# Kernel optimization log

Hardware: AMD Instinct MI355X
Metric: run time of the kernel (lower is better)

The kernel has to match this reference:

```python
import jax, jax.numpy as jnp
import numpy as np

B, T, IN_DIM = 128, 4096, 13
UNITS, MOTOR = 64, 6
LAYERS = [35, 23, 6]   # AutoNCP(64, 6): inter / command / motor neurons
_SPLITS = [35, 58]     # cumulative layer boundaries inside the 64-unit state


def setup_inputs() -> dict:
    keys = iter(jax.random.split(jax.random.key(0), 64))
    def rn(shape, s=0.1):
        return jax.random.normal(next(keys), shape, dtype=jnp.float32) * s
    inp = {"x": jax.random.normal(next(keys), (B, T, IN_DIM), dtype=jnp.float32)}
    # mixed-memory LSTM cell (ncps: input_map has bias, recurrent_map does not)
    inp["lstm_wi"] = rn((4 * UNITS, IN_DIM))
    inp["lstm_wh"] = rn((4 * UNITS, UNITS))
    inp["lstm_b"] = rn((4 * UNITS,))
    # wired CfC layers: ff1/ff2/time_a/time_b acting on concat([input, h])
    in_dims = [IN_DIM] + LAYERS[:-1]
    for i, (d, h) in enumerate(zip(in_dims, LAYERS)):
        for nm in ("w1", "w2", "wa", "wb"):
            inp[f"cfc{i}_{nm}"] = rn((h, d + h))
        for nm in ("b1", "b2", "ba", "bb"):
            inp[f"cfc{i}_{nm}"] = rn((h,))
    inp["gyro_w1"] = rn((32, MOTOR)); inp["gyro_b1"] = rn((32,))
    inp["gyro_w2"] = rn((3, 32));     inp["gyro_b2"] = rn((3,))
    inp["acc_w1"] = rn((32, MOTOR));  inp["acc_b1"] = rn((32,))
    inp["acc_w2"] = rn((3, 32));      inp["acc_b2"] = rn((3,))
    inp["unc_w1"] = rn((16, MOTOR));  inp["unc_b1"] = rn((16,))
    inp["unc_w2"] = rn((6, 16));      inp["unc_b2"] = rn((6,))
    return inp


def _cfc_step(inp, h, p):
    """ncps CfCCell, mode='default', no backbone, ts = 1.0."""
    W1, b1, W2, b2, Wa, ba, Wb, bb = p
    z = jnp.concatenate([inp, h], axis=-1)            # (B, in+hid)
    ff1 = jnp.tanh(z @ W1.T + b1)
    ff2 = jnp.tanh(z @ W2.T + b2)
    t = jax.nn.sigmoid((z @ Wa.T + ba) + (z @ Wb.T + bb))  # t_a*ts + t_b, ts==1
    return ff1 * (1.0 - t) + t * ff2


def reference(x, lstm_wi, lstm_wh, lstm_b,
              cfc0_w1, cfc0_b1, cfc0_w2, cfc0_b2, cfc0_wa, cfc0_ba, cfc0_wb, cfc0_bb,
              cfc1_w1, cfc1_b1, cfc1_w2, cfc1_b2, cfc1_wa, cfc1_ba, cfc1_wb, cfc1_bb,
              cfc2_w1, cfc2_b1, cfc2_w2, cfc2_b2, cfc2_wa, cfc2_ba, cfc2_wb, cfc2_bb,
              gyro_w1, gyro_b1, gyro_w2, gyro_b2,
              acc_w1, acc_b1, acc_w2, acc_b2,
              unc_w1, unc_b1, unc_w2, unc_b2):
    layer_params = (
        (cfc0_w1, cfc0_b1, cfc0_w2, cfc0_b2, cfc0_wa, cfc0_ba, cfc0_wb, cfc0_bb),
        (cfc1_w1, cfc1_b1, cfc1_w2, cfc1_b2, cfc1_wa, cfc1_ba, cfc1_wb, cfc1_bb),
        (cfc2_w1, cfc2_b1, cfc2_w2, cfc2_b2, cfc2_wa, cfc2_ba, cfc2_wb, cfc2_bb),
    )

    def step(carry, xt):  # xt: (B, 13)
        h, c = carry
        # mixed-memory LSTM over the full 64-unit state (forget gate +1.0)
        zg = xt @ lstm_wi.T + lstm_b + h @ lstm_wh.T
        ia, ig, fg, og = jnp.split(zg, 4, axis=-1)
        c_new = c * jax.nn.sigmoid(fg + 1.0) + jnp.tanh(ia) * jax.nn.sigmoid(ig)
        h_lstm = jnp.tanh(c_new) * jax.nn.sigmoid(og)
        # wired CfC: inter -> command -> motor, each fed previous layer's output
        hs = jnp.split(h_lstm, _SPLITS, axis=-1)
        inp = xt
        new_hs = []
        for hi, p in zip(hs, layer_params):
            inp = _cfc_step(inp, hi, p)
            new_hs.append(inp)
        return (jnp.concatenate(new_hs, axis=-1), c_new), inp  # motor out (B,6)

    Bsz = x.shape[0]
    h0 = jnp.zeros((Bsz, UNITS), x.dtype)
    c0 = jnp.zeros((Bsz, UNITS), x.dtype)
    _, outs = jax.lax.scan(step, (h0, c0), jnp.swapaxes(x, 0, 1))
    cfc_out = jnp.swapaxes(outs, 0, 1)  # (B, T, 6)

    gyro = jnp.tanh(cfc_out @ gyro_w1.T + gyro_b1) @ gyro_w2.T + gyro_b2
    acc = jnp.tanh(cfc_out @ acc_w1.T + acc_b1) @ acc_w2.T + acc_b2
    pred = jnp.concatenate([gyro, acc], axis=-1)                      # (B, T, 6)
    unc = jax.nn.softplus(
        jax.nn.relu(cfc_out @ unc_w1.T + unc_b1) @ unc_w2.T + unc_b2)  # (B, T, 6)
    return pred, unc
```

## Files before the change

### kernel.cpp

```cpp
#include <hip/hip_runtime.h>
#include <math.h>

#define BATCH 128
#define TSTEPS 4096
#define INDIM 13
#define XT 64


__device__ __forceinline__ float fsig(float x) {
    return __builtin_amdgcn_rcpf(1.f + __expf(-x));
}
__device__ __forceinline__ float ftanh(float x) {
    float s = fsig(x + x);
    return s + s - 1.f;
}
__device__ __forceinline__ float fsoftplus(float x) {
    return (x > 15.f) ? x : __logf(1.f + __expf(x));
}

__device__ __forceinline__ float qxor1(float v) {
    return __int_as_float(__builtin_amdgcn_update_dpp(
        0, __float_as_int(v), 0xB1, 0xF, 0xF, true));
}
__device__ __forceinline__ float qxor2(float v) {
    return __int_as_float(__builtin_amdgcn_update_dpp(
        0, __float_as_int(v), 0x4E, 0xF, 0xF, true));
}
#define BFLY4(a) { a += qxor1(a); a += qxor2(a); }

#define FMA4(acc, W, q, zv) { acc += zv.x * W##_##q##_0; acc += zv.y * W##_##q##_1; \
                              acc += zv.z * W##_##q##_2; acc += zv.w * W##_##q##_3; }

__global__ __launch_bounds__(256, 1)
void rnn_kernel(const float* __restrict__ x,
                const float* __restrict__ lstm_wi, const float* __restrict__ lstm_wh,
                const float* __restrict__ lstm_b,
                const float* __restrict__ c0w1, const float* __restrict__ c0w2,
                const float* __restrict__ c0wa, const float* __restrict__ c0wb,
                const float* __restrict__ c0b1, const float* __restrict__ c0b2,
                const float* __restrict__ c0ba, const float* __restrict__ c0bb,
                const float* __restrict__ c1w1, const float* __restrict__ c1w2,
                const float* __restrict__ c1wa, const float* __restrict__ c1wb,
                const float* __restrict__ c1b1, const float* __restrict__ c1b2,
                const float* __restrict__ c1ba, const float* __restrict__ c1bb,
                const float* __restrict__ c2w1, const float* __restrict__ c2w2,
                const float* __restrict__ c2wa, const float* __restrict__ c2wb,
                const float* __restrict__ c2b1, const float* __restrict__ c2b2,
                const float* __restrict__ c2ba, const float* __restrict__ c2bb,
                float* __restrict__ out)
{
    const int bb = blockIdx.x;
    const int t  = threadIdx.x;
    const int k  = t & 3;
    const int u  = t >> 2;

    __shared__ __align__(16) float smem[2688];
    float* zL  = smem;
    float* z0  = smem + 96;
    float* z1  = smem + 160;
    float* z2  = smem + 224;
    float* xt0 = smem + 256;
    float* xt1 = smem + 1088;
    float* ot0 = smem + 1920;
    float* ot1 = smem + 2304;

    const long xbase = (long)bb * TSTEPS * INDIM;
    const long obase = (long)bb * TSTEPS * 6;

    auto lwf = [&](int A, int c) -> float {
        int r = A * 64 + u;
        return (c < 13) ? lstm_wi[r * 13 + c]
             : (c < 77) ? lstm_wh[r * 64 + (c - 13)] : 0.f;
    };
#define DEF_WL(A,q) \
    float wl##A##_##q##_0 = lwf(A, 24*k + 4*q + 0); \
    float wl##A##_##q##_1 = lwf(A, 24*k + 4*q + 1); \
    float wl##A##_##q##_2 = lwf(A, 24*k + 4*q + 2); \
    float wl##A##_##q##_3 = lwf(A, 24*k + 4*q + 3);
    DEF_WL(0,0) DEF_WL(0,1) DEF_WL(0,2) DEF_WL(0,3) DEF_WL(0,4) DEF_WL(0,5)
    DEF_WL(1,0) DEF_WL(1,1) DEF_WL(1,2) DEF_WL(1,3) DEF_WL(1,4) DEF_WL(1,5)
    DEF_WL(2,0) DEF_WL(2,1) DEF_WL(2,2) DEF_WL(2,3) DEF_WL(2,4) DEF_WL(2,5)
    DEF_WL(3,0) DEF_WL(3,1) DEF_WL(3,2) DEF_WL(3,3) DEF_WL(3,4) DEF_WL(3,5)
#undef DEF_WL
    const float bL0 = lstm_b[u];
    const float bL1 = lstm_b[64 + u];
    const float bL2 = lstm_b[128 + u];
    const float bL3 = lstm_b[192 + u];

    const int grp  = (u < 35) ? 0 : (u < 58) ? 1 : 2;
    const int row  = (grp == 0) ? u : (grp == 1) ? (u - 35) : (u - 58);
    const int rl   = (grp == 0) ? 48 : (grp == 1) ? 58 : 29;
    const int clen = (grp == 0) ? 12 : (grp == 1) ? 16 : 8;
    const int cb   = clen * k;
    const float *W0p, *W1p, *W2p, *W3p;
    float bC0, bC1, bC2, bC3;
    if (grp == 0) {
        W0p = c0w1 + row * 48; W1p = c0w2 + row * 48;
        W2p = c0wa + row * 48; W3p = c0wb + row * 48;
        bC0 = c0b1[row]; bC1 = c0b2[row]; bC2 = c0ba[row]; bC3 = c0bb[row];
    } else if (grp == 1) {
        W0p = c1w1 + row * 58; W1p = c1w2 + row * 58;
        W2p = c1wa + row * 58; W3p = c1wb + row * 58;
        bC0 = c1b1[row]; bC1 = c1b2[row]; bC2 = c1ba[row]; bC3 = c1bb[row];
    } else {
        W0p = c2w1 + row * 29; W1p = c2w2 + row * 29;
        W2p = c2wa + row * 29; W3p = c2wb + row * 29;
        bC0 = c2b1[row]; bC1 = c2b2[row]; bC2 = c2ba[row]; bC3 = c2bb[row];
    }
    auto cwf = [&](const float* W, int c) -> float {
        int cc = cb + c;
        return (c < clen && cc < rl) ? W[cc] : 0.f;
    };
#define DEF_WC(A,q) \
    float wc##A##_##q##_0 = cwf(W##A##p, 4*q + 0); \
    float wc##A##_##q##_1 = cwf(W##A##p, 4*q + 1); \
    float wc##A##_##q##_2 = cwf(W##A##p, 4*q + 2); \
    float wc##A##_##q##_3 = cwf(W##A##p, 4*q + 3);
    DEF_WC(0,0) DEF_WC(0,1) DEF_WC(0,2) DEF_WC(0,3)
    DEF_WC(1,0) DEF_WC(1,1) DEF_WC(1,2) DEF_WC(1,3)
    DEF_WC(2,0) DEF_WC(2,1) DEF_WC(2,2) DEF_WC(2,3)
    DEF_WC(3,0) DEF_WC(3,1) DEF_WC(3,2) DEF_WC(3,3)
#undef DEF_WC

    float creg = 0.f;

    smem[t] = 0.f;
    if (t < 208) {
        float4 xi = *(const float4*)(x + xbase + 4 * t);
        *(float4*)&xt0[4 * t] = xi;
    }
    if (t < 13) { float x0 = x[xbase + t]; zL[t] = x0; z0[t] = x0; }
    __syncthreads();

    #pragma unroll 1
    for (int ts = 0; ts < TSTEPS; ++ts) {
        const int par = (ts >> 6) & 1;
        const int lts = ts & 63;

        {
            const float4* zc = (const float4*)(zL + 24 * k);
            float4 q0 = zc[0], q1 = zc[1], q2 = zc[2],
                   q3 = zc[3], q4 = zc[4], q5 = zc[5];
            float a0 = 0.f, a1 = 0.f, a2 = 0.f, a3 = 0.f;
            FMA4(a0, wl0, 0, q0) FMA4(a0, wl0, 1, q1) FMA4(a0, wl0, 2, q2)
            FMA4(a0, wl0, 3, q3) FMA4(a0, wl0, 4, q4) FMA4(a0, wl0, 5, q5)
            FMA4(a1, wl1, 0, q0) FMA4(a1, wl1, 1, q1) FMA4(a1, wl1, 2, q2)
            FMA4(a1, wl1, 3, q3) FMA4(a1, wl1, 4, q4) FMA4(a1, wl1, 5, q5)
            FMA4(a2, wl2, 0, q0) FMA4(a2, wl2, 1, q1) FMA4(a2, wl2, 2, q2)
            FMA4(a2, wl2, 3, q3) FMA4(a2, wl2, 4, q4) FMA4(a2, wl2, 5, q5)
            FMA4(a3, wl3, 0, q0) FMA4(a3, wl3, 1, q1) FMA4(a3, wl3, 2, q2)
            FMA4(a3, wl3, 3, q3) FMA4(a3, wl3, 4, q4) FMA4(a3, wl3, 5, q5)
            BFLY4(a0) BFLY4(a1) BFLY4(a2) BFLY4(a3)
            a0 += bL0; a1 += bL1; a2 += bL2; a3 += bL3;
            float cn = creg * fsig(a2 + 1.f) + ftanh(a0) * fsig(a1);
            creg = cn;
            float hl = ftanh(cn) * fsig(a3);
            if (k == 0) {
                if (u < 35)      z0[13 + u] = hl;
                else if (u < 58) z1[u]      = hl;
                else             z2[u - 35] = hl;
            }
        }
        __syncthreads();

        if (grp == 0) {
            const float4* zc = (const float4*)(z0 + 12 * k);
            float4 v0 = zc[0], v1 = zc[1], v2 = zc[2];
            float a0 = 0.f, a1 = 0.f, a2 = 0.f, a3 = 0.f;
            FMA4(a0, wc0, 0, v0) FMA4(a0, wc0, 1, v1) FMA4(a0, wc0, 2, v2)
            FMA4(a1, wc1, 0, v0) FMA4(a1, wc1, 1, v1) FMA4(a1, wc1, 2, v2)
            FMA4(a2, wc2, 0, v0) FMA4(a2, wc2, 1, v1) FMA4(a2, wc2, 2, v2)
            FMA4(a3, wc3, 0, v0) FMA4(a3, wc3, 1, v1) FMA4(a3, wc3, 2, v2)
            BFLY4(a0) BFLY4(a1) BFLY4(a2) BFLY4(a3)
            a0 += bC0; a1 += bC1; a2 += bC2; a3 += bC3;
            float tg = fsig(a2 + a3);
            float f1 = ftanh(a0), f2 = ftanh(a1);
            float o = f1 + tg * (f2 - f1);
            if (k == 0) { z1[row] = o; zL[13 + row] = o; }
        } else {
            if (lts == 62 && (ts + 2) < TSTEPS) {
                int i = (t - 140) * 2;
                float* dst = par ? xt0 : xt1;
                const float* src = x + xbase + (long)(ts + 2) * 13;
                if (i < 208)     *(float4*)&dst[4*i]     = *(const float4*)(src + 4*i);
                if (i + 1 < 208) *(float4*)&dst[4*(i+1)] = *(const float4*)(src + 4*(i+1));
            }
            if (lts == 0 && ts > 0) {
                int i = t - 140;
                if (i < 96) {
                    const float* src = par ? ot0 : ot1;
                    float4 v = *(const float4*)&src[4 * i];
                    *(float4*)(out + obase + (long)(ts - XT) * 6 + 4 * i) = v;
                }
            }
        }
        __syncthreads();

        if (grp == 1) {
            const float4* zc = (const float4*)(z1 + 16 * k);
            float4 v0 = zc[0], v1 = zc[1], v2 = zc[2], v3 = zc[3];
            float a0 = 0.f, a1 = 0.f, a2 = 0.f, a3 = 0.f;
            FMA4(a0, wc0, 0, v0) FMA4(a0, wc0, 1, v1) FMA4(a0, wc0, 2, v2) FMA4(a0, wc0, 3, v3)
            FMA4(a1, wc1, 0, v0) FMA4(a1, wc1, 1, v1) FMA4(a1, wc1, 2, v2) FMA4(a1, wc1, 3, v3)
            FMA4(a2, wc2, 0, v0) FMA4(a2, wc2, 1, v1) FMA4(a2, wc2, 2, v2) FMA4(a2, wc2, 3, v3)
            FMA4(a3, wc3, 0, v0) FMA4(a3, wc3, 1, v1) FMA4(a3, wc3, 2, v2) FMA4(a3, wc3, 3, v3)
            BFLY4(a0) BFLY4(a1) BFLY4(a2) BFLY4(a3)
            a0 += bC0; a1 += bC1; a2 += bC2; a3 += bC3;
            float tg = fsig(a2 + a3);
            float f1 = ftanh(a0), f2 = ftanh(a1);
            float o = f1 + tg * (f2 - f1);
            if (k == 0) { z2[row] = o; zL[48 + row] = o; }
        }
        __syncthreads();

        if (grp == 2) {
            const float4* zc = (const float4*)(z2 + 8 * k);
            float4 v0 = zc[0], v1 = zc[1];
            float a0 = 0.f, a1 = 0.f, a2 = 0.f, a3 = 0.f;
            FMA4(a0, wc0, 0, v0) FMA4(a0, wc0, 1, v1)
            FMA4(a1, wc1, 0, v0) FMA4(a1, wc1, 1, v1)
            FMA4(a2, wc2, 0, v0) FMA4(a2, wc2, 1, v1)
            FMA4(a3, wc3, 0, v0) FMA4(a3, wc3, 1, v1)
            BFLY4(a0) BFLY4(a1) BFLY4(a2) BFLY4(a3)
            a0 += bC0; a1 += bC1; a2 += bC2; a3 += bC3;
            float tg = fsig(a2 + a3);
            float f1 = ftanh(a0), f2 = ftanh(a1);
            float o = f1 + tg * (f2 - f1);
            if (k == 0) {
                zL[71 + row] = o;
                float* ob = par ? ot1 : ot0;
                ob[lts * 6 + row] = o;
            }
        } else if (t < 13 && (ts + 1) < TSTEPS) {
            const float* xb = (((ts + 1) >> 6) & 1) ? xt1 : xt0;
            float xn = xb[((ts + 1) & 63) * 13 + t];
            zL[t] = xn; z0[t] = xn;
        }
        __syncthreads();
    }

    if (t < 96) {
        float4 v = *(const float4*)&ot1[4 * t];
        *(float4*)(out + obase + (long)(TSTEPS - XT) * 6 + 4 * t) = v;
    }
}

#define S_GW1 0
#define S_GB1 192
#define S_GW2 224
#define S_GB2 320
#define S_AW1 323
#define S_AB1 515
#define S_AW2 547
#define S_AB2 643
#define S_UW1 646
#define S_UB1 742
#define S_UW2 758
#define S_UB2 854
#define S_TOT 860

__global__ __launch_bounds__(256)
void head_kernel(const float* __restrict__ gw1, const float* __restrict__ gb1,
                 const float* __restrict__ gw2, const float* __restrict__ gb2,
                 const float* __restrict__ aw1, const float* __restrict__ ab1,
                 const float* __restrict__ aw2, const float* __restrict__ ab2,
                 const float* __restrict__ uw1, const float* __restrict__ ub1,
                 const float* __restrict__ uw2, const float* __restrict__ ub2,
                 float* __restrict__ out)
{
    __shared__ float s[S_TOT];
    const int t = threadIdx.x;
    if (t < 192) { s[S_GW1 + t] = gw1[t]; s[S_AW1 + t] = aw1[t]; }
    if (t < 96)  { s[S_GW2 + t] = gw2[t]; s[S_AW2 + t] = aw2[t];
                   s[S_UW1 + t] = uw1[t]; s[S_UW2 + t] = uw2[t]; }
    if (t < 32)  { s[S_GB1 + t] = gb1[t]; s[S_AB1 + t] = ab1[t]; }
    if (t < 16)  { s[S_UB1 + t] = ub1[t]; }
    if (t < 3)   { s[S_GB2 + t] = gb2[t]; s[S_AB2 + t] = ab2[t]; }
    if (t < 6)   { s[S_UB2 + t] = ub2[t]; }
    __syncthreads();

    const long p = (long)blockIdx.x * 256 + t;
    const long base = p * 6;
    float m0 = out[base+0], m1 = out[base+1], m2 = out[base+2];
    float m3 = out[base+3], m4 = out[base+4], m5 = out[base+5];

    float gy0 = s[S_GB2+0], gy1 = s[S_GB2+1], gy2 = s[S_GB2+2];
    float ac0 = s[S_AB2+0], ac1 = s[S_AB2+1], ac2 = s[S_AB2+2];
    #pragma unroll
    for (int i = 0; i < 32; ++i) {
        float hg = s[S_GB1+i] + s[S_GW1+i*6+0]*m0 + s[S_GW1+i*6+1]*m1
                 + s[S_GW1+i*6+2]*m2 + s[S_GW1+i*6+3]*m3
                 + s[S_GW1+i*6+4]*m4 + s[S_GW1+i*6+5]*m5;
        hg = ftanh(hg);
        gy0 += s[S_GW2+i]*hg; gy1 += s[S_GW2+32+i]*hg; gy2 += s[S_GW2+64+i]*hg;
        float ha = s[S_AB1+i] + s[S_AW1+i*6+0]*m0 + s[S_AW1+i*6+1]*m1
                 + s[S_AW1+i*6+2]*m2 + s[S_AW1+i*6+3]*m3
                 + s[S_AW1+i*6+4]*m4 + s[S_AW1+i*6+5]*m5;
        ha = ftanh(ha);
        ac0 += s[S_AW2+i]*ha; ac1 += s[S_AW2+32+i]*ha; ac2 += s[S_AW2+64+i]*ha;
    }
    float u0 = s[S_UB2+0], u1 = s[S_UB2+1], u2 = s[S_UB2+2];
    float u3 = s[S_UB2+3], u4 = s[S_UB2+4], u5 = s[S_UB2+5];
    #pragma unroll
    for (int i = 0; i < 16; ++i) {
        float hu = s[S_UB1+i] + s[S_UW1+i*6+0]*m0 + s[S_UW1+i*6+1]*m1
                 + s[S_UW1+i*6+2]*m2 + s[S_UW1+i*6+3]*m3
                 + s[S_UW1+i*6+4]*m4 + s[S_UW1+i*6+5]*m5;
        hu = fmaxf(hu, 0.f);
        u0 += s[S_UW2+i]*hu;      u1 += s[S_UW2+16+i]*hu; u2 += s[S_UW2+32+i]*hu;
        u3 += s[S_UW2+48+i]*hu;   u4 += s[S_UW2+64+i]*hu; u5 += s[S_UW2+80+i]*hu;
    }
    out[base+0] = gy0; out[base+1] = gy1; out[base+2] = gy2;
    out[base+3] = ac0; out[base+4] = ac1; out[base+5] = ac2;
    const long uoff = (long)BATCH * TSTEPS * 6;
    out[uoff+base+0] = fsoftplus(u0); out[uoff+base+1] = fsoftplus(u1);
    out[uoff+base+2] = fsoftplus(u2); out[uoff+base+3] = fsoftplus(u3);
    out[uoff+base+4] = fsoftplus(u4); out[uoff+base+5] = fsoftplus(u5);
}

extern "C" void kernel_launch(void* const* d_in, const int* in_sizes, int n_in,
                              void* d_out, int out_size, void* d_ws, size_t ws_size,
                              hipStream_t stream) {
    const float* x       = (const float*)d_in[0];
    const float* lstm_wi = (const float*)d_in[1];
    const float* lstm_wh = (const float*)d_in[2];
    const float* lstm_b  = (const float*)d_in[3];
    const float* c0w1 = (const float*)d_in[4];
    const float* c0w2 = (const float*)d_in[5];
    const float* c0wa = (const float*)d_in[6];
    const float* c0wb = (const float*)d_in[7];
    const float* c0b1 = (const float*)d_in[8];
    const float* c0b2 = (const float*)d_in[9];
    const float* c0ba = (const float*)d_in[10];
    const float* c0bb = (const float*)d_in[11];
    const float* c1w1 = (const float*)d_in[12];
    const float* c1w2 = (const float*)d_in[13];
    const float* c1wa = (const float*)d_in[14];
    const float* c1wb = (const float*)d_in[15];
    const float* c1b1 = (const float*)d_in[16];
    const float* c1b2 = (const float*)d_in[17];
    const float* c1ba = (const float*)d_in[18];
    const float* c1bb = (const float*)d_in[19];
    const float* c2w1 = (const float*)d_in[20];
    const float* c2w2 = (const float*)d_in[21];
    const float* c2wa = (const float*)d_in[22];
    const float* c2wb = (const float*)d_in[23];
    const float* c2b1 = (const float*)d_in[24];
    const float* c2b2 = (const float*)d_in[25];
    const float* c2ba = (const float*)d_in[26];
    const float* c2bb = (const float*)d_in[27];
    const float* gw1 = (const float*)d_in[28];
    const float* gb1 = (const float*)d_in[29];
    const float* gw2 = (const float*)d_in[30];
    const float* gb2 = (const float*)d_in[31];
    const float* aw1 = (const float*)d_in[32];
    const float* ab1 = (const float*)d_in[33];
    const float* aw2 = (const float*)d_in[34];
    const float* ab2 = (const float*)d_in[35];
    const float* uw1 = (const float*)d_in[36];
    const float* ub1 = (const float*)d_in[37];
    const float* uw2 = (const float*)d_in[38];
    const float* ub2 = (const float*)d_in[39];
    float* out = (float*)d_out;

    rnn_kernel<<<BATCH, 256, 0, stream>>>(x, lstm_wi, lstm_wh, lstm_b,
        c0w1, c0w2, c0wa, c0wb, c0b1, c0b2, c0ba, c0bb,
        c1w1, c1w2, c1wa, c1wb, c1b1, c1b2, c1ba, c1bb,
        c2w1, c2w2, c2wa, c2wb, c2b1, c2b2, c2ba, c2bb, out);

    head_kernel<<<(BATCH * TSTEPS) / 256, 256, 0, stream>>>(
        gw1, gb1, gw2, gb2, aw1, ab1, aw2, ab2, uw1, ub1, uw2, ub2, out);
}
```

Before: 5.327 ms.

## Replace block-wide barriers with wave-specialized flag-synchronized pipeline across LSTM and CfC stages

```diff
diff --git a/kernel.cpp b/kernel.cpp
--- a/kernel.cpp
+++ b/kernel.cpp
@@ -4,8 +4,31 @@
 #define BATCH 128
 #define TSTEPS 4096
 #define INDIM 13
-#define XT 64
-
+
+
+#define FLG_PS1 16
+#define FLG_PS2 528
+#define FLG_PS3 1040
+#define FLG_PS4 1552
+#define OFF_HB  2064
+#define OFF_O0  2192
+#define OFF_O1  2264
+#define OFF_O2  2336
+#define OFF_XT0 2352
+#define OFF_XT1 3184
+#define OFF_OT0 4016
+#define OFF_OT1 4400
+#define STOT    4784
+
+#define F_P0 0
+#define F_P1 1
+#define F_P2 2
+#define F_H  3
+#define F_O0 4
+#define F_O1 5
+#define F_O2 6
+#define F_A1 7
+#define F_A2 8
 
 __device__ __forceinline__ float fsig(float x) {
     return __builtin_amdgcn_rcpf(1.f + __expf(-x));
@@ -18,18 +41,28 @@
     return (x > 15.f) ? x : __logf(1.f + __expf(x));
 }
 
-__device__ __forceinline__ float qxor1(float v) {
-    return __int_as_float(__builtin_amdgcn_update_dpp(
-        0, __float_as_int(v), 0xB1, 0xF, 0xF, true));
-}
-__device__ __forceinline__ float qxor2(float v) {
-    return __int_as_float(__builtin_amdgcn_update_dpp(
-        0, __float_as_int(v), 0x4E, 0xF, 0xF, true));
-}
-#define BFLY4(a) { a += qxor1(a); a += qxor2(a); }
-
-#define FMA4(acc, W, q, zv) { acc += zv.x * W##_##q##_0; acc += zv.y * W##_##q##_1; \
-                              acc += zv.z * W##_##q##_2; acc += zv.w * W##_##q##_3; }
+#define FENCE() { asm volatile("s_waitcnt lgkmcnt(0)" ::: "memory"); \
+                  __builtin_amdgcn_sched_barrier(0); }
+#define PUBLISH(F, V) { FENCE(); if (l == 0) flg[F] = (V); }
+#define POLL(F, V) { while (flg[F] < (V)) {} __builtin_amdgcn_sched_barrier(0); }
+
+#define STAGE36(OUT, OPOFF, POFF) float OUT; { \
+    const float4* _q = (const float4*)(smem + (OPOFF)); \
+    float4 _v0=_q[0],_v1=_q[1],_v2=_q[2],_v3=_q[3],_v4=_q[4], \
+           _v5=_q[5],_v6=_q[6],_v7=_q[7],_v8=_q[8]; \
+    float4 _P = *(const float4*)(smem + (POFF) + 4*l); \
+    float _op[36] = {_v0.x,_v0.y,_v0.z,_v0.w,_v1.x,_v1.y,_v1.z,_v1.w, \
+                     _v2.x,_v2.y,_v2.z,_v2.w,_v3.x,_v3.y,_v3.z,_v3.w, \
+                     _v4.x,_v4.y,_v4.z,_v4.w,_v5.x,_v5.y,_v5.z,_v5.w, \
+                     _v6.x,_v6.y,_v6.z,_v6.w,_v7.x,_v7.y,_v7.z,_v7.w, \
+                     _v8.x,_v8.y,_v8.z,_v8.w}; \
+    float _a0=_P.x,_a1=_P.y,_a2=_P.z,_a3=_P.w; \
+    _Pragma("unroll") \
+    for (int _j = 0; _j < 36; ++_j) { \
+        _a0 += _op[_j]*wcA[0][_j]; _a1 += _op[_j]*wcA[1][_j]; \
+        _a2 += _op[_j]*wcA[2][_j]; _a3 += _op[_j]*wcA[3][_j]; } \
+    float _tg = fsig(_a2+_a3), _f1 = ftanh(_a0), _f2 = ftanh(_a1); \
+    OUT = _f1 + _tg*(_f2-_f1); }
 
 __global__ __launch_bounds__(256, 1)
 void rnn_kernel(const float* __restrict__ x,
@@ -49,199 +82,378 @@
                 const float* __restrict__ c2ba, const float* __restrict__ c2bb,
                 float* __restrict__ out)
 {
-    const int bb = blockIdx.x;
-    const int t  = threadIdx.x;
-    const int k  = t & 3;
-    const int u  = t >> 2;
-
-    __shared__ __align__(16) float smem[2688];
-    float* zL  = smem;
-    float* z0  = smem + 96;
-    float* z1  = smem + 160;
-    float* z2  = smem + 224;
-    float* xt0 = smem + 256;
-    float* xt1 = smem + 1088;
-    float* ot0 = smem + 1920;
-    float* ot1 = smem + 2304;
-
-    const long xbase = (long)bb * TSTEPS * INDIM;
-    const long obase = (long)bb * TSTEPS * 6;
-
-    auto lwf = [&](int A, int c) -> float {
-        int r = A * 64 + u;
-        return (c < 13) ? lstm_wi[r * 13 + c]
-             : (c < 77) ? lstm_wh[r * 64 + (c - 13)] : 0.f;
-    };
-#define DEF_WL(A,q) \
-    float wl##A##_##q##_0 = lwf(A, 24*k + 4*q + 0); \
-    float wl##A##_##q##_1 = lwf(A, 24*k + 4*q + 1); \
-    float wl##A##_##q##_2 = lwf(A, 24*k + 4*q + 2); \
-    float wl##A##_##q##_3 = lwf(A, 24*k + 4*q + 3);
-    DEF_WL(0,0) DEF_WL(0,1) DEF_WL(0,2) DEF_WL(0,3) DEF_WL(0,4) DEF_WL(0,5)
-    DEF_WL(1,0) DEF_WL(1,1) DEF_WL(1,2) DEF_WL(1,3) DEF_WL(1,4) DEF_WL(1,5)
-    DEF_WL(2,0) DEF_WL(2,1) DEF_WL(2,2) DEF_WL(2,3) DEF_WL(2,4) DEF_WL(2,5)
-    DEF_WL(3,0) DEF_WL(3,1) DEF_WL(3,2) DEF_WL(3,3) DEF_WL(3,4) DEF_WL(3,5)
-#undef DEF_WL
-    const float bL0 = lstm_b[u];
-    const float bL1 = lstm_b[64 + u];
-    const float bL2 = lstm_b[128 + u];
-    const float bL3 = lstm_b[192 + u];
-
-    const int grp  = (u < 35) ? 0 : (u < 58) ? 1 : 2;
-    const int row  = (grp == 0) ? u : (grp == 1) ? (u - 35) : (u - 58);
-    const int rl   = (grp == 0) ? 48 : (grp == 1) ? 58 : 29;
-    const int clen = (grp == 0) ? 12 : (grp == 1) ? 16 : 8;
-    const int cb   = clen * k;
-    const float *W0p, *W1p, *W2p, *W3p;
-    float bC0, bC1, bC2, bC3;
-    if (grp == 0) {
-        W0p = c0w1 + row * 48; W1p = c0w2 + row * 48;
-        W2p = c0wa + row * 48; W3p = c0wb + row * 48;
-        bC0 = c0b1[row]; bC1 = c0b2[row]; bC2 = c0ba[row]; bC3 = c0bb[row];
-    } else if (grp == 1) {
-        W0p = c1w1 + row * 58; W1p = c1w2 + row * 58;
-        W2p = c1wa + row * 58; W3p = c1wb + row * 58;
-        bC0 = c1b1[row]; bC1 = c1b2[row]; bC2 = c1ba[row]; bC3 = c1bb[row];
-    } else {
-        W0p = c2w1 + row * 29; W1p = c2w2 + row * 29;
-        W2p = c2wa + row * 29; W3p = c2wb + row * 29;
-        bC0 = c2b1[row]; bC1 = c2b2[row]; bC2 = c2ba[row]; bC3 = c2bb[row];
-    }
-    auto cwf = [&](const float* W, int c) -> float {
-        int cc = cb + c;
-        return (c < clen && cc < rl) ? W[cc] : 0.f;
-    };
-#define DEF_WC(A,q) \
-    float wc##A##_##q##_0 = cwf(W##A##p, 4*q + 0); \
-    float wc##A##_##q##_1 = cwf(W##A##p, 4*q + 1); \
-    float wc##A##_##q##_2 = cwf(W##A##p, 4*q + 2); \
-    float wc##A##_##q##_3 = cwf(W##A##p, 4*q + 3);
-    DEF_WC(0,0) DEF_WC(0,1) DEF_WC(0,2) DEF_WC(0,3)
-    DEF_WC(1,0) DEF_WC(1,1) DEF_WC(1,2) DEF_WC(1,3)
-    DEF_WC(2,0) DEF_WC(2,1) DEF_WC(2,2) DEF_WC(2,3)
-    DEF_WC(3,0) DEF_WC(3,1) DEF_WC(3,2) DEF_WC(3,3)
-#undef DEF_WC
-
-    float creg = 0.f;
-
-    smem[t] = 0.f;
+    const int t = threadIdx.x;
+    const int l = t & 63;
+    const int w = t >> 6;
+
+    __shared__ __align__(16) float smem[STOT];
+    volatile int* flg = (volatile int*)smem;
+
+    const long xbase = (long)blockIdx.x * TSTEPS * INDIM;
+    const long obase = (long)blockIdx.x * TSTEPS * 6;
+
+    for (int i = t; i < OFF_XT0; i += 256) smem[i] = 0.f;
     if (t < 208) {
         float4 xi = *(const float4*)(x + xbase + 4 * t);
-        *(float4*)&xt0[4 * t] = xi;
+        *(float4*)&smem[OFF_XT0 + 4 * t] = xi;
     }
-    if (t < 13) { float x0 = x[xbase + t]; zL[t] = x0; z0[t] = x0; }
     __syncthreads();
-
-    #pragma unroll 1
-    for (int ts = 0; ts < TSTEPS; ++ts) {
-        const int par = (ts >> 6) & 1;
-        const int lts = ts & 63;
-
+    if (t == 0) {
+        #pragma unroll
+        for (int i = 0; i < 9; ++i) flg[i] = -1;
+    }
+    __syncthreads();
+
+    if (w == 0) {
+        float wlA[4][6];
+        #pragma unroll
+        for (int g = 0; g < 4; ++g)
+            #pragma unroll
+            for (int j = 0; j < 6; ++j)
+                wlA[g][j] = lstm_wh[((g << 6) + l) * 64 + 58 + j];
+        float wcA[4][36];
+        #pragma unroll
+        for (int g = 0; g < 4; ++g)
+            #pragma unroll
+            for (int j = 0; j < 36; ++j) wcA[g][j] = 0.f;
+        if (l < 35) {
+            #pragma unroll
+            for (int g = 0; g < 4; ++g) {
+                const float* W = (g==0)?c0w1:(g==1)?c0w2:(g==2)?c0wa:c0wb;
+                #pragma unroll
+                for (int j = 0; j < 35; ++j) wcA[g][j] = W[l*48 + 13 + j];
+            }
+        } else if (l < 58) {
+            const int r = l - 35;
+            #pragma unroll
+            for (int g = 0; g < 4; ++g) {
+                const float* W = (g==0)?c1w1:(g==1)?c1w2:(g==2)?c1wa:c1wb;
+                #pragma unroll
+                for (int j = 0; j < 35; ++j) wcA[g][j] = W[r*58 + j];
+            }
+        } else {
+            const int r = l - 58;
+            #pragma unroll
+            for (int g = 0; g < 4; ++g) {
+                const float* W = (g==0)?c2w1:(g==1)?c2w2:(g==2)?c2wa:c2wb;
+                #pragma unroll
+                for (int j = 0; j < 23; ++j) wcA[g][j] = W[r*29 + j];
+            }
+        }
+        float creg = 0.f;
+
+        #pragma unroll 1
+        for (int ts = 0; ts < TSTEPS; ++ts) {
+            const int par = ts & 1, nxt = par ^ 1;
+            { while (flg[F_P0] < ts || flg[F_P1] < ts || flg[F_P2] < ts) {} }
+            __builtin_amdgcn_sched_barrier(0);
+            {
+                float4 P  = *(const float4*)(smem + FLG_PS1 + par*256 + 4*l);
+                float4 oa = *(const float4*)(smem + OFF_O2 + par*8);
+                float2 ob = *(const float2*)(smem + OFF_O2 + par*8 + 4);
+                float o2v[6] = {oa.x, oa.y, oa.z, oa.w, ob.x, ob.y};
+                float a0 = P.x, a1 = P.y, a2 = P.z, a3 = P.w;
+                #pragma unroll
+                for (int j = 0; j < 6; ++j) {
+                    a0 += o2v[j]*wlA[0][j]; a1 += o2v[j]*wlA[1][j];
+                    a2 += o2v[j]*wlA[2][j]; a3 += o2v[j]*wlA[3][j];
+                }
+                float cn = creg * fsig(a2 + 1.f) + ftanh(a0) * fsig(a1);
+                creg = cn;
+                float hv = ftanh(cn) * fsig(a3);
+                smem[OFF_HB + par*64 + l] = hv;
+            }
+            PUBLISH(F_H, ts);
+            STAGE36(oS2, OFF_HB + par*64, FLG_PS2 + par*256);
+            if (l < 35) smem[OFF_O0 + par*36 + l] = oS2;
+            PUBLISH(F_O0, ts);
+            POLL(F_A1, ts);
+            STAGE36(oS3, OFF_O0 + par*36, FLG_PS3 + par*256);
+            if (l >= 35 && l < 58) smem[OFF_O1 + par*36 + (l - 35)] = oS3;
+            PUBLISH(F_O1, ts);
+            POLL(F_A2, ts);
+            STAGE36(oS4, OFF_O1 + par*36, FLG_PS4 + par*256);
+            if (l >= 58) smem[OFF_O2 + nxt*8 + (l - 58)] = oS4;
+            PUBLISH(F_O2, ts);
+        }
+    } else if (w == 1) {
+        const int u = l >> 2, g = l & 3;
+        float wbx[13], wbo0[36], wbo1[24];
+        #pragma unroll
+        for (int j = 0; j < 13; ++j) wbx[j] = lstm_wi[(g*64 + u)*13 + j];
+        #pragma unroll
+        for (int j = 0; j < 36; ++j) wbo0[j] = (j < 35) ? lstm_wh[(g*64 + u)*64 + j] : 0.f;
+        #pragma unroll
+        for (int j = 0; j < 24; ++j) wbo1[j] = (j < 23) ? lstm_wh[(g*64 + u)*64 + 35 + j] : 0.f;
+        const float bb = lstm_b[g*64 + u];
+        const int r0 = l >> 2, g0 = l & 3;
+        const int p1v = (l < 28);
+        const int r1 = (l + 64) >> 2, g1 = l & 3;
+        float wA0[28], wA1[28];
         {
-            const float4* zc = (const float4*)(zL + 24 * k);
-            float4 q0 = zc[0], q1 = zc[1], q2 = zc[2],
-                   q3 = zc[3], q4 = zc[4], q5 = zc[5];
-            float a0 = 0.f, a1 = 0.f, a2 = 0.f, a3 = 0.f;
-            FMA4(a0, wl0, 0, q0) FMA4(a0, wl0, 1, q1) FMA4(a0, wl0, 2, q2)
-            FMA4(a0, wl0, 3, q3) FMA4(a0, wl0, 4, q4) FMA4(a0, wl0, 5, q5)
-            FMA4(a1, wl1, 0, q0) FMA4(a1, wl1, 1, q1) FMA4(a1, wl1, 2, q2)
-            FMA4(a1, wl1, 3, q3) FMA4(a1, wl1, 4, q4) FMA4(a1, wl1, 5, q5)
-            FMA4(a2, wl2, 0, q0) FMA4(a2, wl2, 1, q1) FMA4(a2, wl2, 2, q2)
-            FMA4(a2, wl2, 3, q3) FMA4(a2, wl2, 4, q4) FMA4(a2, wl2, 5, q5)
-            FMA4(a3, wl3, 0, q0) FMA4(a3, wl3, 1, q1) FMA4(a3, wl3, 2, q2)
-            FMA4(a3, wl3, 3, q3) FMA4(a3, wl3, 4, q4) FMA4(a3, wl3, 5, q5)
-            BFLY4(a0) BFLY4(a1) BFLY4(a2) BFLY4(a3)
-            a0 += bL0; a1 += bL1; a2 += bL2; a3 += bL3;
-            float cn = creg * fsig(a2 + 1.f) + ftanh(a0) * fsig(a1);
-            creg = cn;
-            float hl = ftanh(cn) * fsig(a3);
-            if (k == 0) {
-                if (u < 35)      z0[13 + u] = hl;
-                else if (u < 58) z1[u]      = hl;
-                else             z2[u - 35] = hl;
-            }
-        }
-        __syncthreads();
-
-        if (grp == 0) {
-            const float4* zc = (const float4*)(z0 + 12 * k);
-            float4 v0 = zc[0], v1 = zc[1], v2 = zc[2];
-            float a0 = 0.f, a1 = 0.f, a2 = 0.f, a3 = 0.f;
-            FMA4(a0, wc0, 0, v0) FMA4(a0, wc0, 1, v1) FMA4(a0, wc0, 2, v2)
-            FMA4(a1, wc1, 0, v0) FMA4(a1, wc1, 1, v1) FMA4(a1, wc1, 2, v2)
-            FMA4(a2, wc2, 0, v0) FMA4(a2, wc2, 1, v1) FMA4(a2, wc2, 2, v2)
-            FMA4(a3, wc3, 0, v0) FMA4(a3, wc3, 1, v1) FMA4(a3, wc3, 2, v2)
-            BFLY4(a0) BFLY4(a1) BFLY4(a2) BFLY4(a3)
-            a0 += bC0; a1 += bC1; a2 += bC2; a3 += bC3;
-            float tg = fsig(a2 + a3);
-            float f1 = ftanh(a0), f2 = ftanh(a1);
-            float o = f1 + tg * (f2 - f1);
-            if (k == 0) { z1[row] = o; zL[13 + row] = o; }
-        } else {
-            if (lts == 62 && (ts + 2) < TSTEPS) {
-                int i = (t - 140) * 2;
-                float* dst = par ? xt0 : xt1;
-                const float* src = x + xbase + (long)(ts + 2) * 13;
-                if (i < 208)     *(float4*)&dst[4*i]     = *(const float4*)(src + 4*i);
-                if (i + 1 < 208) *(float4*)&dst[4*(i+1)] = *(const float4*)(src + 4*(i+1));
-            }
-            if (lts == 0 && ts > 0) {
-                int i = t - 140;
-                if (i < 96) {
-                    const float* src = par ? ot0 : ot1;
-                    float4 v = *(const float4*)&src[4 * i];
-                    *(float4*)(out + obase + (long)(ts - XT) * 6 + 4 * i) = v;
+            const float* W0 = (g0==0)?c1w1:(g0==1)?c1w2:(g0==2)?c1wa:c1wb;
+            #pragma unroll
+            for (int j = 0; j < 28; ++j)
+                wA0[j] = (j >= 3 && j < 26) ? W0[r0*58 + 32 + j] : 0.f;
+            const float* W1 = (g1==0)?c1w1:(g1==1)?c1w2:(g1==2)?c1wa:c1wb;
+            #pragma unroll
+            for (int j = 0; j < 28; ++j)
+                wA1[j] = (p1v && j >= 3 && j < 26) ? W1[r1*58 + 32 + j] : 0.f;
+        }
+        const float ba0 = ((g0==0)?c1b1:(g0==1)?c1b2:(g0==2)?c1ba:c1bb)[r0];
+        const float ba1 = p1v ? ((g1==0)?c1b1:(g1==1)?c1b2:(g1==2)?c1ba:c1bb)[r1] : 0.f;
+
+        #pragma unroll 1
+        for (int ts = 0; ts < TSTEPS; ++ts) {
+            const int par = ts & 1, prv = par ^ 1;
+            POLL(F_O0, ts - 1);
+            const float* xr = smem + (((ts >> 6) & 1) ? OFF_XT1 : OFF_XT0) + (ts & 63)*13;
+            float a = bb;
+            #pragma unroll
+            for (int j = 0; j < 13; ++j) a += xr[j] * wbx[j];
+            {
+                const float4* q = (const float4*)(smem + OFF_O0 + prv*36);
+                float4 v0=q[0],v1=q[1],v2=q[2],v3=q[3],v4=q[4],v5=q[5],v6=q[6],v7=q[7],v8=q[8];
+                float ov[36] = {v0.x,v0.y,v0.z,v0.w,v1.x,v1.y,v1.z,v1.w,
+                                v2.x,v2.y,v2.z,v2.w,v3.x,v3.y,v3.z,v3.w,
+                                v4.x,v4.y,v4.z,v4.w,v5.x,v5.y,v5.z,v5.w,
+                                v6.x,v6.y,v6.z,v6.w,v7.x,v7.y,v7.z,v7.w,
+                                v8.x,v8.y,v8.z,v8.w};
+                #pragma unroll
+                for (int j = 0; j < 36; ++j) a += ov[j] * wbo0[j];
+            }
+            POLL(F_O1, ts - 1);
+            {
+                const float4* q = (const float4*)(smem + OFF_O1 + prv*36);
+                float4 v0=q[0],v1=q[1],v2=q[2],v3=q[3],v4=q[4],v5=q[5];
+                float ov[24] = {v0.x,v0.y,v0.z,v0.w,v1.x,v1.y,v1.z,v1.w,
+                                v2.x,v2.y,v2.z,v2.w,v3.x,v3.y,v3.z,v3.w,
+                                v4.x,v4.y,v4.z,v4.w,v5.x,v5.y,v5.z,v5.w};
+                #pragma unroll
+                for (int j = 0; j < 24; ++j) a += ov[j] * wbo1[j];
+            }
+            smem[FLG_PS1 + par*256 + l] = a;
+            PUBLISH(F_P0, ts);
+            POLL(F_H, ts);
+            {
+                const float4* q = (const float4*)(smem + OFF_HB + par*64 + 32);
+                float4 v0=q[0],v1=q[1],v2=q[2],v3=q[3],v4=q[4],v5=q[5],v6=q[6];
+                float hv[28] = {v0.x,v0.y,v0.z,v0.w,v1.x,v1.y,v1.z,v1.w,
+                                v2.x,v2.y,v2.z,v2.w,v3.x,v3.y,v3.z,v3.w,
+                                v4.x,v4.y,v4.z,v4.w,v5.x,v5.y,v5.z,v5.w,
+                                v6.x,v6.y,v6.z,v6.w};
+                float A0 = ba0, A1 = ba1;
+                #pragma unroll
+                for (int j = 0; j < 28; ++j) { A0 += hv[j]*wA0[j]; A1 += hv[j]*wA1[j]; }
+                smem[FLG_PS3 + par*256 + 140 + l] = A0;
+                if (p1v) smem[FLG_PS3 + par*256 + 140 + 64 + l] = A1;
+            }
+            PUBLISH(F_A1, ts);
+        }
+    } else if (w == 2) {
+        const int u = 16 + (l >> 2), g = l & 3;
+        float wbx[13], wbo0[36], wbo1[24];
+        #pragma unroll
+        for (int j = 0; j < 13; ++j) wbx[j] = lstm_wi[(g*64 + u)*13 + j];
+        #pragma unroll
+        for (int j = 0; j < 36; ++j) wbo0[j] = (j < 35) ? lstm_wh[(g*64 + u)*64 + j] : 0.f;
+        #pragma unroll
+        for (int j = 0; j < 24; ++j) wbo1[j] = (j < 23) ? lstm_wh[(g*64 + u)*64 + 35 + j] : 0.f;
+        const float bb = lstm_b[g*64 + u];
+        float wX0[13], wX1[13], wX2[13];
+        float bx0, bx1, bx2;
+        {
+            const int r = l >> 2, gg = l & 3;
+            const float* W = (gg==0)?c0w1:(gg==1)?c0w2:(gg==2)?c0wa:c0wb;
+            #pragma unroll
+            for (int j = 0; j < 13; ++j) wX0[j] = W[r*48 + j];
+            bx0 = ((gg==0)?c0b1:(gg==1)?c0b2:(gg==2)?c0ba:c0bb)[r];
+        }
+        {
+            const int r = (64 + l) >> 2, gg = l & 3;
+            const float* W = (gg==0)?c0w1:(gg==1)?c0w2:(gg==2)?c0wa:c0wb;
+            #pragma unroll
+            for (int j = 0; j < 13; ++j) wX1[j] = W[r*48 + j];
+            bx1 = ((gg==0)?c0b1:(gg==1)?c0b2:(gg==2)?c0ba:c0bb)[r];
+        }
+        {
+            const int ok = (l < 12);
+            const int r = ok ? ((128 + l) >> 2) : 0, gg = l & 3;
+            const float* W = (gg==0)?c0w1:(gg==1)?c0w2:(gg==2)?c0wa:c0wb;
+            #pragma unroll
+            for (int j = 0; j < 13; ++j) wX2[j] = ok ? W[r*48 + j] : 0.f;
+            bx2 = ok ? ((gg==0)?c0b1:(gg==1)?c0b2:(gg==2)?c0ba:c0bb)[r] : 0.f;
+        }
+        float wC[8]; float bc2 = 0.f;
+        {
+            const int ok = (l < 24);
+            const int r = ok ? (l >> 2) : 0, gg = l & 3;
+            const float* W = (gg==0)?c2w1:(gg==1)?c2w2:(gg==2)?c2wa:c2wb;
+            #pragma unroll
+            for (int j = 0; j < 8; ++j)
+                wC[j] = (ok && j >= 2) ? W[r*29 + 21 + j] : 0.f;
+            bc2 = ok ? ((gg==0)?c2b1:(gg==1)?c2b2:(gg==2)?c2ba:c2bb)[r] : 0.f;
+        }
+
+        #pragma unroll 1
+        for (int ts = 0; ts < TSTEPS; ++ts) {
+            const int par = ts & 1, prv = par ^ 1;
+            POLL(F_O0, ts - 1);
+            const float* xr = smem + (((ts >> 6) & 1) ? OFF_XT1 : OFF_XT0) + (ts & 63)*13;
+            float xv[13];
+            #pragma unroll
+            for (int j = 0; j < 13; ++j) xv[j] = xr[j];
+            float cx0 = bx0, cx1 = bx1, cx2 = bx2;
+            #pragma unroll
+            for (int j = 0; j < 13; ++j) {
+                cx0 += xv[j]*wX0[j]; cx1 += xv[j]*wX1[j]; cx2 += xv[j]*wX2[j];
+            }
+            smem[FLG_PS2 + par*256 + l] = cx0;
+            smem[FLG_PS2 + par*256 + 64 + l] = cx1;
+            if (l < 12) smem[FLG_PS2 + par*256 + 128 + l] = cx2;
+            float a = bb;
+            #pragma unroll
+            for (int j = 0; j < 13; ++j) a += xv[j] * wbx[j];
+            {
+                const float4* q = (const float4*)(smem + OFF_O0 + prv*36);
+                float4 v0=q[0],v1=q[1],v2=q[2],v3=q[3],v4=q[4],v5=q[5],v6=q[6],v7=q[7],v8=q[8];
+                float ov[36] = {v0.x,v0.y,v0.z,v0.w,v1.x,v1.y,v1.z,v1.w,
+                                v2.x,v2.y,v2.z,v2.w,v3.x,v3.y,v3.z,v3.w,
+                                v4.x,v4.y,v4.z,v4.w,v5.x,v5.y,v5.z,v5.w,
+                                v6.x,v6.y,v6.z,v6.w,v7.x,v7.y,v7.z,v7.w,
+                                v8.x,v8.y,v8.z,v8.w};
+                #pragma unroll
+                for (int j = 0; j < 36; ++j) a += ov[j] * wbo0[j];
+            }
+            POLL(F_O1, ts - 1);
+            {
+                const float4* q = (const float4*)(smem + OFF_O1 + prv*36);
+                float4 v0=q[0],v1=q[1],v2=q[2],v3=q[3],v4=q[4],v5=q[5];
+                float ov[24] = {v0.x,v0.y,v0.z,v0.w,v1.x,v1.y,v1.z,v1.w,
+                                v2.x,v2.y,v2.z,v2.w,v3.x,v3.y,v3.z,v3.w,
+                                v4.x,v4.y,v4.z,v4.w,v5.x,v5.y,v5.z,v5.w};
+                #pragma unroll
+                for (int j = 0; j < 24; ++j) a += ov[j] * wbo1[j];
+            }
+            smem[FLG_PS1 + par*256 + 64 + l] = a;
+            PUBLISH(F_P1, ts);
+            POLL(F_H, ts);
+            if (l < 24) {
+                const float2* q = (const float2*)(smem + OFF_HB + par*64 + 56);
+                float2 h0 = q[0], h1 = q[1], h2 = q[2], h3 = q[3];
+                float hv[8] = {h0.x,h0.y,h1.x,h1.y,h2.x,h2.y,h3.x,h3.y};
+                float A = bc2;
+                #pragma unroll
+                for (int j = 0; j < 8; ++j) A += hv[j]*wC[j];
+                smem[FLG_PS4 + par*256 + 232 + l] = A;
+            }
+            PUBLISH(F_A2, ts);
+            if (ts > 0) {
+                POLL(F_O2, ts - 1);
+                const int rp = ts - 1, tp = (rp >> 6) & 1;
+                if (l < 6)
+                    smem[(tp ? OFF_OT1 : OFF_OT0) + (rp & 63)*6 + l] =
+                        smem[OFF_O2 + (ts & 1)*8 + l];
+                if ((ts & 63) == 0) {
+                    FENCE();
+                    const float* otb = smem + (tp ? OFF_OT1 : OFF_OT0);
+                    float4 v = ((const float4*)otb)[l];
+                    *(float4*)(out + obase + (long)(ts - 64)*6 + 4*l) = v;
+                    if (l < 32) {
+                        float4 v2 = ((const float4*)otb)[64 + l];
+                        *(float4*)(out + obase + (long)(ts - 64)*6 + 256 + 4*l) = v2;
+                    }
                 }
             }
         }
-        __syncthreads();
-
-        if (grp == 1) {
-            const float4* zc = (const float4*)(z1 + 16 * k);
-            float4 v0 = zc[0], v1 = zc[1], v2 = zc[2], v3 = zc[3];
-            float a0 = 0.f, a1 = 0.f, a2 = 0.f, a3 = 0.f;
-            FMA4(a0, wc0, 0, v0) FMA4(a0, wc0, 1, v1) FMA4(a0, wc0, 2, v2) FMA4(a0, wc0, 3, v3)
-            FMA4(a1, wc1, 0, v0) FMA4(a1, wc1, 1, v1) FMA4(a1, wc1, 2, v2) FMA4(a1, wc1, 3, v3)
-            FMA4(a2, wc2, 0, v0) FMA4(a2, wc2, 1, v1) FMA4(a2, wc2, 2, v2) FMA4(a2, wc2, 3, v3)
-            FMA4(a3, wc3, 0, v0) FMA4(a3, wc3, 1, v1) FMA4(a3, wc3, 2, v2) FMA4(a3, wc3, 3, v3)
-            BFLY4(a0) BFLY4(a1) BFLY4(a2) BFLY4(a3)
-            a0 += bC0; a1 += bC1; a2 += bC2; a3 += bC3;
-            float tg = fsig(a2 + a3);
-            float f1 = ftanh(a0), f2 = ftanh(a1);
-            float o = f1 + tg * (f2 - f1);
-            if (k == 0) { z2[row] = o; zL[48 + row] = o; }
-        }
-        __syncthreads();
-
-        if (grp == 2) {
-            const float4* zc = (const float4*)(z2 + 8 * k);
-            float4 v0 = zc[0], v1 = zc[1];
-            float a0 = 0.f, a1 = 0.f, a2 = 0.f, a3 = 0.f;
-            FMA4(a0, wc0, 0, v0) FMA4(a0, wc0, 1, v1)
-            FMA4(a1, wc1, 0, v0) FMA4(a1, wc1, 1, v1)
-            FMA4(a2, wc2, 0, v0) FMA4(a2, wc2, 1, v1)
-            FMA4(a3, wc3, 0, v0) FMA4(a3, wc3, 1, v1)
-            BFLY4(a0) BFLY4(a1) BFLY4(a2) BFLY4(a3)
-            a0 += bC0; a1 += bC1; a2 += bC2; a3 += bC3;
-            float tg = fsig(a2 + a3);
-            float f1 = ftanh(a0), f2 = ftanh(a1);
-            float o = f1 + tg * (f2 - f1);
-            if (k == 0) {
-                zL[71 + row] = o;
-                float* ob = par ? ot1 : ot0;
-                ob[lts * 6 + row] = o;
-            }
-        } else if (t < 13 && (ts + 1) < TSTEPS) {
-            const float* xb = (((ts + 1) >> 6) & 1) ? xt1 : xt0;
-            float xn = xb[((ts + 1) & 63) * 13 + t];
-            zL[t] = xn; z0[t] = xn;
-        }
-        __syncthreads();
-    }
-
-    if (t < 96) {
-        float4 v = *(const float4*)&ot1[4 * t];
-        *(float4*)(out + obase + (long)(TSTEPS - XT) * 6 + 4 * t) = v;
+        POLL(F_O2, TSTEPS - 1);
+        if (l < 6)
+            smem[OFF_OT1 + 63*6 + l] = smem[OFF_O2 + 0*8 + l];
+        FENCE();
+        {
+            const float* otb = smem + OFF_OT1;
+            float4 v = ((const float4*)otb)[l];
+            *(float4*)(out + obase + (long)(TSTEPS - 64)*6 + 4*l) = v;
+            if (l < 32) {
+                float4 v2 = ((const float4*)otb)[64 + l];
+                *(float4*)(out + obase + (long)(TSTEPS - 64)*6 + 256 + 4*l) = v2;
+            }
+        }
+    } else {
+        const int g = l & 3;
+        const int u0 = 32 + (l >> 2), u1 = 48 + (l >> 2);
+        float wbx0[13], wbo00[36], wbo10[24];
+        float wbx1[13], wbo01[36], wbo11[24];
+        #pragma unroll
+        for (int j = 0; j < 13; ++j) {
+            wbx0[j] = lstm_wi[(g*64 + u0)*13 + j];
+            wbx1[j] = lstm_wi[(g*64 + u1)*13 + j];
+        }
+        #pragma unroll
+        for (int j = 0; j < 36; ++j) {
+            wbo00[j] = (j < 35) ? lstm_wh[(g*64 + u0)*64 + j] : 0.f;
+            wbo01[j] = (j < 35) ? lstm_wh[(g*64 + u1)*64 + j] : 0.f;
+        }
+        #pragma unroll
+        for (int j = 0; j < 24; ++j) {
+            wbo10[j] = (j < 23) ? lstm_wh[(g*64 + u0)*64 + 35 + j] : 0.f;
+            wbo11[j] = (j < 23) ? lstm_wh[(g*64 + u1)*64 + 35 + j] : 0.f;
+        }
+        const float bb0 = lstm_b[g*64 + u0];
+        const float bb1 = lstm_b[g*64 + u1];
+
+        #pragma unroll 1
+        for (int ts = 0; ts < TSTEPS; ++ts) {
+            const int par = ts & 1, prv = par ^ 1;
+            float4 r0, r1, r2, r3;
+            const bool doref = ((ts & 63) == 62) && (ts + 2) < TSTEPS;
+            if (doref) {
+                const float* src = x + xbase + (long)(ts + 2)*13;
+                if (4*l + 0 < 208) r0 = *(const float4*)(src + 4*(4*l + 0));
+                if (4*l + 1 < 208) r1 = *(const float4*)(src + 4*(4*l + 1));
+                if (4*l + 2 < 208) r2 = *(const float4*)(src + 4*(4*l + 2));
+                if (4*l + 3 < 208) r3 = *(const float4*)(src + 4*(4*l + 3));
+            }
+            POLL(F_O0, ts - 1);
+            const float* xr = smem + (((ts >> 6) & 1) ? OFF_XT1 : OFF_XT0) + (ts & 63)*13;
+            float xv[13];
+            #pragma unroll
+            for (int j = 0; j < 13; ++j) xv[j] = xr[j];
+            float a = bb0, b = bb1;
+            #pragma unroll
+            for (int j = 0; j < 13; ++j) { a += xv[j]*wbx0[j]; b += xv[j]*wbx1[j]; }
+            {
+                const float4* q = (const float4*)(smem + OFF_O0 + prv*36);
+                float4 v0=q[0],v1=q[1],v2=q[2],v3=q[3],v4=q[4],v5=q[5],v6=q[6],v7=q[7],v8=q[8];
+                float ov[36] = {v0.x,v0.y,v0.z,v0.w,v1.x,v1.y,v1.z,v1.w,
+                                v2.x,v2.y,v2.z,v2.w,v3.x,v3.y,v3.z,v3.w,
+                                v4.x,v4.y,v4.z,v4.w,v5.x,v5.y,v5.z,v5.w,
+                                v6.x,v6.y,v6.z,v6.w,v7.x,v7.y,v7.z,v7.w,
+                                v8.x,v8.y,v8.z,v8.w};
+                #pragma unroll
+                for (int j = 0; j < 36; ++j) { a += ov[j]*wbo00[j]; b += ov[j]*wbo01[j]; }
+            }
+            POLL(F_O1, ts - 1);
+            {
+                const float4* q = (const float4*)(smem + OFF_O1 + prv*36);
+                float4 v0=q[0],v1=q[1],v2=q[2],v3=q[3],v4=q[4],v5=q[5];
+                float ov[24] = {v0.x,v0.y,v0.z,v0.w,v1.x,v1.y,v1.z,v1.w,
+                                v2.x,v2.y,v2.z,v2.w,v3.x,v3.y,v3.z,v3.w,
+                                v4.x,v4.y,v4.z,v4.w,v5.x,v5.y,v5.z,v5.w};
+                #pragma unroll
+                for (int j = 0; j < 24; ++j) { a += ov[j]*wbo10[j]; b += ov[j]*wbo11[j]; }
+            }
+            smem[FLG_PS1 + par*256 + 128 + l] = a;
+            smem[FLG_PS1 + par*256 + 192 + l] = b;
+            if (doref) {
+                float* dst = smem + (((ts >> 6) & 1) ? OFF_XT0 : OFF_XT1);
+                if (4*l + 0 < 208) *(float4*)(dst + 4*(4*l + 0)) = r0;
+                if (4*l + 1 < 208) *(float4*)(dst + 4*(4*l + 1)) = r1;
+                if (4*l + 2 < 208) *(float4*)(dst + 4*(4*l + 2)) = r2;
+                if (4*l + 3 < 208) *(float4*)(dst + 4*(4*l + 3)) = r3;
+            }
+            PUBLISH(F_P2, ts);
+        }
     }
 }
 
```

Result: slower. 9.019 ms (+69.3%).
